# Kernel tuning notes

Hardware: AMD Instinct MI355X
Metric: run time of the kernel (lower is better)

## Reference

```python
import jax, jax.numpy as jnp
import numpy as np

# SMPL kinematic tree, first 22 joints (root has parent -1)
PARENTS = [-1, 0, 0, 0, 1, 2, 3, 4, 5, 6, 7, 8, 9, 9, 9, 12, 13, 14, 16, 17, 18, 19]
B, L, J = 64, 2048, 22


def axis_angle_to_matrix(aa):
    """aa: (..., 3) axis-angle -> (..., 3, 3) rotation matrix (Rodrigues)."""
    sq = jnp.sum(aa * aa, axis=-1, keepdims=True)
    angle = jnp.sqrt(sq + 1e-12)
    axis = aa / angle
    x, y, z = axis[..., 0], axis[..., 1], axis[..., 2]
    ang = angle[..., 0]
    c, s = jnp.cos(ang), jnp.sin(ang)
    t = 1.0 - c
    R = jnp.stack([
        t * x * x + c,     t * x * y - s * z, t * x * z + s * y,
        t * x * y + s * z, t * y * y + c,     t * y * z - s * x,
        t * x * z - s * y, t * y * z + s * x, t * z * z + c,
    ], axis=-1)
    return R.reshape(aa.shape[:-1] + (3, 3))


def get_TRS(rotmat, pos):
    """rotmat (...,3,3), pos (...,3) -> homogeneous (...,4,4)."""
    top = jnp.concatenate([rotmat, pos[..., :, None]], axis=-1)  # (...,3,4)
    bottom = jnp.broadcast_to(
        jnp.array([0.0, 0.0, 0.0, 1.0], rotmat.dtype), top.shape[:-2] + (1, 4))
    return jnp.concatenate([top, bottom], axis=-2)


def forward_kinematics(mat, parents):
    """mat: (B,L,J,4,4) local transforms -> global transforms via parent chain."""
    out = [mat[:, :, 0]]
    for j in range(1, mat.shape[2]):
        out.append(out[parents[j]] @ mat[:, :, j])
    return jnp.stack(out, axis=2)


def setup_inputs() -> dict:
    key = jax.random.key(0)
    ks = jax.random.split(key, 6)
    return {
        "body_pose": 0.3 * jax.random.normal(ks[0], (B, L, 63), jnp.float32),
        "betas": jax.random.normal(ks[1], (B, L, 10), jnp.float32),
        "global_orient": 0.3 * jax.random.normal(ks[2], (B, L, 3), jnp.float32),
        "transl": jax.random.normal(ks[3], (B, L, 3), jnp.float32),
        "J_template": jax.random.normal(ks[4], (J, 3), jnp.float32),
        "J_shapedirs": 0.01 * jax.random.normal(ks[5], (J, 3, 10), jnp.float32),
    }


def reference(body_pose, betas, global_orient, transl, J_template, J_shapedirs):
    Bm, Lm = body_pose.shape[:2]
    # (B,L,22,3) axis-angle: global orient + 21 body joints
    aa = jnp.concatenate([global_orient, body_pose], axis=-1).reshape(Bm, Lm, -1, 3)
    rotmat = axis_angle_to_matrix(aa)                                  # (B,L,22,3,3)
    skeleton = J_template[None, None] + jnp.einsum('blk,jck->bljc', betas, J_shapedirs)
    # local offsets: child - parent, root keeps its own position (+ transl)
    parent_idx = jnp.array([0] + PARENTS[1:])
    local = skeleton - skeleton[:, :, parent_idx]
    local = local.at[:, :, 0].set(skeleton[:, :, 0] + transl)
    mat = get_TRS(rotmat, local)                                       # (B,L,22,4,4)
    fk_mat = forward_kinematics(mat, PARENTS)                          # (B,L,22,4,4)
    joints = fk_mat[..., :3, 3]                                        # (B,L,22,3)
    return joints
```

## Files before the change

### kernel.cpp

```cpp
#include <hip/hip_runtime.h>

#define NT 128
#define NJ 22

struct X9 { float r[9]; float t[3]; };

__device__ __forceinline__ void rodrigues(float ax, float ay, float az, float* R) {
    float sq   = ax*ax + ay*ay + az*az + 1e-12f;
    float rinv = rsqrtf(sq);
    float ang  = sq * rinv;
    float s, c;
    __sincosf(ang, &s, &c);
    float x = ax*rinv, y = ay*rinv, z = az*rinv;
    float t = 1.0f - c;
    R[0] = t*x*x + c;   R[1] = t*x*y - s*z; R[2] = t*x*z + s*y;
    R[3] = t*x*y + s*z; R[4] = t*y*y + c;   R[5] = t*y*z - s*x;
    R[6] = t*x*z - s*y; R[7] = t*y*z + s*x; R[8] = t*z*z + c;
}

__device__ __forceinline__ void local_pos(int j, const float* bt,
                                          const float* LT, const float4* LD4,
                                          float* lt) {
    #pragma unroll
    for (int c = 0; c < 3; ++c) {
        float v = LT[j*3 + c];
        const float4 a0 = LD4[(j*3 + c)*3 + 0];
        const float4 a1 = LD4[(j*3 + c)*3 + 1];
        const float4 a2 = LD4[(j*3 + c)*3 + 2];
        v = fmaf(bt[0], a0.x, v); v = fmaf(bt[1], a0.y, v);
        v = fmaf(bt[2], a0.z, v); v = fmaf(bt[3], a0.w, v);
        v = fmaf(bt[4], a1.x, v); v = fmaf(bt[5], a1.y, v);
        v = fmaf(bt[6], a1.z, v); v = fmaf(bt[7], a1.w, v);
        v = fmaf(bt[8], a2.x, v); v = fmaf(bt[9], a2.y, v);
        lt[c] = v;
    }
}

template<int J>
__device__ __forceinline__ X9 step(const X9& gp, float* bp, const float* bt,
                                   const float* LT, const float4* LD4) {
    float R[9];
    rodrigues(bp[(J-1)*3 + 0], bp[(J-1)*3 + 1], bp[(J-1)*3 + 2], R);
    float lt[3];
    local_pos(J, bt, LT, LD4, lt);
    X9 g;
    #pragma unroll
    for (int r = 0; r < 3; ++r) {
        #pragma unroll
        for (int c = 0; c < 3; ++c)
            g.r[r*3+c] = fmaf(gp.r[r*3+0], R[c],
                         fmaf(gp.r[r*3+1], R[3+c],
                              gp.r[r*3+2] * R[6+c]));
        g.t[r] = fmaf(gp.r[r*3+0], lt[0],
                 fmaf(gp.r[r*3+1], lt[1],
                 fmaf(gp.r[r*3+2], lt[2], gp.t[r])));
    }
    bp[(J-1)*3+0] = g.t[0]; bp[(J-1)*3+1] = g.t[1]; bp[(J-1)*3+2] = g.t[2];
    return g;
}

__global__ __launch_bounds__(NT) void fk_joints_kernel(
    const float* __restrict__ body_pose,
    const float* __restrict__ betas,
    const float* __restrict__ global_orient,
    const float* __restrict__ transl,
    const float* __restrict__ J_template,
    const float* __restrict__ J_shapedirs,
    float* __restrict__ out)
{
    __shared__ float  s_bp[NT*63];
    __shared__ float  s_bt[NT*10];
    __shared__ float  s_go[NT*3];
    __shared__ float  s_tr[NT*3];
    __shared__ float  s_LT[NJ*3];
    __shared__ float4 s_LD4[NJ*3*3];

    const int tid = threadIdx.x;
    const long long s0 = (long long)blockIdx.x * NT;

    {
        const float4* src = reinterpret_cast<const float4*>(body_pose + s0*63);
        float4* dst = reinterpret_cast<float4*>(s_bp);
        #pragma unroll 4
        for (int i = tid; i < NT*63/4; i += NT) dst[i] = src[i];
    }
    {
        const float4* src = reinterpret_cast<const float4*>(betas + s0*10);
        float4* dst = reinterpret_cast<float4*>(s_bt);
        for (int i = tid; i < NT*10/4; i += NT) dst[i] = src[i];
    }
    {
        const float4* src = reinterpret_cast<const float4*>(global_orient + s0*3);
        float4* dst = reinterpret_cast<float4*>(s_go);
        if (tid < NT*3/4) dst[tid] = src[tid];
    }
    {
        const float4* src = reinterpret_cast<const float4*>(transl + s0*3);
        float4* dst = reinterpret_cast<float4*>(s_tr);
        if (tid < NT*3/4) dst[tid] = src[tid];
    }

    const int P[NJ] = {0,0,0,0,1,2,3,4,5,6,7,8,9,9,9,12,13,14,16,17,18,19};
    float* s_LD = reinterpret_cast<float*>(s_LD4);
    for (int i = tid; i < NJ*3; i += NT) {
        int j = i/3, c = i - j*3;
        float v = J_template[i];
        if (j) v -= J_template[P[j]*3 + c];
        s_LT[i] = v;
        s_LD[i*12 + 10] = 0.0f;
        s_LD[i*12 + 11] = 0.0f;
    }
    for (int i = tid; i < NJ*30; i += NT) {
        int jc = i/10, k = i - jc*10;
        int j = jc/3,  c = jc - j*3;
        float v = J_shapedirs[i];
        if (j) v -= J_shapedirs[(P[j]*3 + c)*10 + k];
        s_LD[jc*12 + k] = v;
    }
    __syncthreads();

    float bt[10];
    #pragma unroll
    for (int k = 0; k < 10; ++k) bt[k] = s_bt[tid*10 + k];

    float* bp = &s_bp[tid*63];

    X9 g0;
    rodrigues(s_go[tid*3+0], s_go[tid*3+1], s_go[tid*3+2], g0.r);
    {
        float lt0[3];
        local_pos(0, bt, s_LT, s_LD4, lt0);
        g0.t[0] = lt0[0] + s_tr[tid*3+0];
        g0.t[1] = lt0[1] + s_tr[tid*3+1];
        g0.t[2] = lt0[2] + s_tr[tid*3+2];
        s_go[tid*3+0] = g0.t[0]; s_go[tid*3+1] = g0.t[1]; s_go[tid*3+2] = g0.t[2];
    }

    X9 g;
    g = step<1 >(g0, bp, bt, s_LT, s_LD4);
    g = step<4 >(g,  bp, bt, s_LT, s_LD4);
    g = step<7 >(g,  bp, bt, s_LT, s_LD4);
    g = step<10>(g,  bp, bt, s_LT, s_LD4);
    g = step<2 >(g0, bp, bt, s_LT, s_LD4);
    g = step<5 >(g,  bp, bt, s_LT, s_LD4);
    g = step<8 >(g,  bp, bt, s_LT, s_LD4);
    g = step<11>(g,  bp, bt, s_LT, s_LD4);
    g = step<3 >(g0, bp, bt, s_LT, s_LD4);
    g = step<6 >(g,  bp, bt, s_LT, s_LD4);
    X9 g9 = step<9>(g, bp, bt, s_LT, s_LD4);
    g = step<12>(g9, bp, bt, s_LT, s_LD4);
    g = step<15>(g,  bp, bt, s_LT, s_LD4);
    g = step<13>(g9, bp, bt, s_LT, s_LD4);
    g = step<16>(g,  bp, bt, s_LT, s_LD4);
    g = step<18>(g,  bp, bt, s_LT, s_LD4);
    g = step<20>(g,  bp, bt, s_LT, s_LD4);
    g = step<14>(g9, bp, bt, s_LT, s_LD4);
    g = step<17>(g,  bp, bt, s_LT, s_LD4);
    g = step<19>(g,  bp, bt, s_LT, s_LD4);
    g = step<21>(g,  bp, bt, s_LT, s_LD4);

    __syncthreads();

    {
        float4* dst = reinterpret_cast<float4*>(out + s0 * (NJ*3));
        const int TOT4 = NT*NJ*3/4;
        for (int i = tid; i < TOT4; i += NT) {
            const int f0 = i*4;
            float v[4];
            #pragma unroll
            for (int q = 0; q < 4; ++q) {
                int f = f0 + q;
                int s = f / 66;
                int r = f - s*66;
                v[q] = (r < 3) ? s_go[s*3 + r] : s_bp[s*63 + (r - 3)];
            }
            dst[i] = make_float4(v[0], v[1], v[2], v[3]);
        }
    }
}

extern "C" void kernel_launch(void* const* d_in, const int* in_sizes, int n_in,
                              void* d_out, int out_size, void* d_ws, size_t ws_size,
                              hipStream_t stream) {
    const float* body_pose     = (const float*)d_in[0];
    const float* betas         = (const float*)d_in[1];
    const float* global_orient = (const float*)d_in[2];
    const float* transl        = (const float*)d_in[3];
    const float* J_template    = (const float*)d_in[4];
    const float* J_shapedirs   = (const float*)d_in[5];
    float* out = (float*)d_out;

    const int S = in_sizes[0] / 63;
    const int blocks = S / NT;

    hipLaunchKernelGGL(fk_joints_kernel, dim3(blocks), dim3(NT), 0, stream,
                       body_pose, betas, global_orient, transl,
                       J_template, J_shapedirs, out);
}
```

Measured before the change: 35.68 us.

## Reuse one shared buffer, hold poses in registers, write output contiguously

Shared memory is cut to a single NT*66 buffer that is reused over three phases. Body pose is staged there first and pulled into 63 registers per thread. The buffer then stages betas, global orient and translation, and finally holds the joint outputs in the exact output layout, so the epilogue becomes a plain float4 copy with no per-element div/mod gather. Launch bounds ask for 2 blocks per SM. The goal is lower LDS usage and simpler stores, paid for with extra barriers and high register pressure from the 63-element array, which may spill.

```diff
diff --git a/kernel.cpp b/kernel.cpp
--- a/kernel.cpp
+++ b/kernel.cpp
@@ -37,10 +37,10 @@
 }
 
 template<int J>
-__device__ __forceinline__ X9 step(const X9& gp, float* bp, const float* bt,
-                                   const float* LT, const float4* LD4) {
+__device__ __forceinline__ X9 step(const X9& gp, const float* aa, const float* bt,
+                                   const float* LT, const float4* LD4, float* s_o) {
     float R[9];
-    rodrigues(bp[(J-1)*3 + 0], bp[(J-1)*3 + 1], bp[(J-1)*3 + 2], R);
+    rodrigues(aa[(J-1)*3 + 0], aa[(J-1)*3 + 1], aa[(J-1)*3 + 2], R);
     float lt[3];
     local_pos(J, bt, LT, LD4, lt);
     X9 g;
@@ -55,11 +55,11 @@
                  fmaf(gp.r[r*3+1], lt[1],
                  fmaf(gp.r[r*3+2], lt[2], gp.t[r])));
     }
-    bp[(J-1)*3+0] = g.t[0]; bp[(J-1)*3+1] = g.t[1]; bp[(J-1)*3+2] = g.t[2];
+    s_o[J*3+0] = g.t[0]; s_o[J*3+1] = g.t[1]; s_o[J*3+2] = g.t[2];
     return g;
 }
 
-__global__ __launch_bounds__(NT) void fk_joints_kernel(
+__global__ __launch_bounds__(NT, 2) void fk_joints_kernel(
     const float* __restrict__ body_pose,
     const float* __restrict__ betas,
     const float* __restrict__ global_orient,
@@ -68,10 +68,7 @@
     const float* __restrict__ J_shapedirs,
     float* __restrict__ out)
 {
-    __shared__ float  s_bp[NT*63];
-    __shared__ float  s_bt[NT*10];
-    __shared__ float  s_go[NT*3];
-    __shared__ float  s_tr[NT*3];
+    __shared__ float  s_buf[NT*66];
     __shared__ float  s_LT[NJ*3];
     __shared__ float4 s_LD4[NJ*3*3];
 
@@ -80,26 +77,9 @@
 
     {
         const float4* src = reinterpret_cast<const float4*>(body_pose + s0*63);
-        float4* dst = reinterpret_cast<float4*>(s_bp);
-        #pragma unroll 4
+        float4* dst = reinterpret_cast<float4*>(s_buf);
         for (int i = tid; i < NT*63/4; i += NT) dst[i] = src[i];
     }
-    {
-        const float4* src = reinterpret_cast<const float4*>(betas + s0*10);
-        float4* dst = reinterpret_cast<float4*>(s_bt);
-        for (int i = tid; i < NT*10/4; i += NT) dst[i] = src[i];
-    }
-    {
-        const float4* src = reinterpret_cast<const float4*>(global_orient + s0*3);
-        float4* dst = reinterpret_cast<float4*>(s_go);
-        if (tid < NT*3/4) dst[tid] = src[tid];
-    }
-    {
-        const float4* src = reinterpret_cast<const float4*>(transl + s0*3);
-        float4* dst = reinterpret_cast<float4*>(s_tr);
-        if (tid < NT*3/4) dst[tid] = src[tid];
-    }
-
     const int P[NJ] = {0,0,0,0,1,2,3,4,5,6,7,8,9,9,9,12,13,14,16,17,18,19};
     float* s_LD = reinterpret_cast<float*>(s_LD4);
     for (int i = tid; i < NJ*3; i += NT) {
@@ -119,63 +99,81 @@
     }
     __syncthreads();
 
+    float aa[63];
+    #pragma unroll
+    for (int k = 0; k < 63; ++k) aa[k] = s_buf[tid*63 + k];
+    __syncthreads();
+
+    {
+        const float4* src = reinterpret_cast<const float4*>(betas + s0*10);
+        float4* dst = reinterpret_cast<float4*>(s_buf);
+        for (int i = tid; i < NT*10/4; i += NT) dst[i] = src[i];
+    }
+    {
+        const float4* src = reinterpret_cast<const float4*>(global_orient + s0*3);
+        float4* dst = reinterpret_cast<float4*>(s_buf + NT*10);
+        if (tid < NT*3/4) dst[tid] = src[tid];
+    }
+    {
+        const float4* src = reinterpret_cast<const float4*>(transl + s0*3);
+        float4* dst = reinterpret_cast<float4*>(s_buf + NT*13);
+        if (tid < NT*3/4) dst[tid] = src[tid];
+    }
+    __syncthreads();
+
     float bt[10];
     #pragma unroll
-    for (int k = 0; k < 10; ++k) bt[k] = s_bt[tid*10 + k];
+    for (int k = 0; k < 10; ++k) bt[k] = s_buf[tid*10 + k];
+    const float gox = s_buf[NT*10 + tid*3 + 0];
+    const float goy = s_buf[NT*10 + tid*3 + 1];
+    const float goz = s_buf[NT*10 + tid*3 + 2];
+    const float trx = s_buf[NT*13 + tid*3 + 0];
+    const float try_ = s_buf[NT*13 + tid*3 + 1];
+    const float trz = s_buf[NT*13 + tid*3 + 2];
+    __syncthreads();
 
-    float* bp = &s_bp[tid*63];
+    float* s_o = &s_buf[tid*66];
 
     X9 g0;
-    rodrigues(s_go[tid*3+0], s_go[tid*3+1], s_go[tid*3+2], g0.r);
+    rodrigues(gox, goy, goz, g0.r);
     {
         float lt0[3];
         local_pos(0, bt, s_LT, s_LD4, lt0);
-        g0.t[0] = lt0[0] + s_tr[tid*3+0];
-        g0.t[1] = lt0[1] + s_tr[tid*3+1];
-        g0.t[2] = lt0[2] + s_tr[tid*3+2];
-        s_go[tid*3+0] = g0.t[0]; s_go[tid*3+1] = g0.t[1]; s_go[tid*3+2] = g0.t[2];
+        g0.t[0] = lt0[0] + trx;
+        g0.t[1] = lt0[1] + try_;
+        g0.t[2] = lt0[2] + trz;
+        s_o[0] = g0.t[0]; s_o[1] = g0.t[1]; s_o[2] = g0.t[2];
     }
 
     X9 g;
-    g = step<1 >(g0, bp, bt, s_LT, s_LD4);
-    g = step<4 >(g,  bp, bt, s_LT, s_LD4);
-    g = step<7 >(g,  bp, bt, s_LT, s_LD4);
-    g = step<10>(g,  bp, bt, s_LT, s_LD4);
-    g = step<2 >(g0, bp, bt, s_LT, s_LD4);
-    g = step<5 >(g,  bp, bt, s_LT, s_LD4);
-    g = step<8 >(g,  bp, bt, s_LT, s_LD4);
-    g = step<11>(g,  bp, bt, s_LT, s_LD4);
-    g = step<3 >(g0, bp, bt, s_LT, s_LD4);
-    g = step<6 >(g,  bp, bt, s_LT, s_LD4);
-    X9 g9 = step<9>(g, bp, bt, s_LT, s_LD4);
-    g = step<12>(g9, bp, bt, s_LT, s_LD4);
-    g = step<15>(g,  bp, bt, s_LT, s_LD4);
-    g = step<13>(g9, bp, bt, s_LT, s_LD4);
-    g = step<16>(g,  bp, bt, s_LT, s_LD4);
-    g = step<18>(g,  bp, bt, s_LT, s_LD4);
-    g = step<20>(g,  bp, bt, s_LT, s_LD4);
-    g = step<14>(g9, bp, bt, s_LT, s_LD4);
-    g = step<17>(g,  bp, bt, s_LT, s_LD4);
-    g = step<19>(g,  bp, bt, s_LT, s_LD4);
-    g = step<21>(g,  bp, bt, s_LT, s_LD4);
+    g = step<1 >(g0, aa, bt, s_LT, s_LD4, s_o);
+    g = step<4 >(g,  aa, bt, s_LT, s_LD4, s_o);
+    g = step<7 >(g,  aa, bt, s_LT, s_LD4, s_o);
+    g = step<10>(g,  aa, bt, s_LT, s_LD4, s_o);
+    g = step<2 >(g0, aa, bt, s_LT, s_LD4, s_o);
+    g = step<5 >(g,  aa, bt, s_LT, s_LD4, s_o);
+    g = step<8 >(g,  aa, bt, s_LT, s_LD4, s_o);
+    g = step<11>(g,  aa, bt, s_LT, s_LD4, s_o);
+    g = step<3 >(g0, aa, bt, s_LT, s_LD4, s_o);
+    g = step<6 >(g,  aa, bt, s_LT, s_LD4, s_o);
+    X9 g9 = step<9>(g, aa, bt, s_LT, s_LD4, s_o);
+    g = step<12>(g9, aa, bt, s_LT, s_LD4, s_o);
+    g = step<15>(g,  aa, bt, s_LT, s_LD4, s_o);
+    g = step<13>(g9, aa, bt, s_LT, s_LD4, s_o);
+    g = step<16>(g,  aa, bt, s_LT, s_LD4, s_o);
+    g = step<18>(g,  aa, bt, s_LT, s_LD4, s_o);
+    g = step<20>(g,  aa, bt, s_LT, s_LD4, s_o);
+    g = step<14>(g9, aa, bt, s_LT, s_LD4, s_o);
+    g = step<17>(g,  aa, bt, s_LT, s_LD4, s_o);
+    g = step<19>(g,  aa, bt, s_LT, s_LD4, s_o);
+    g = step<21>(g,  aa, bt, s_LT, s_LD4, s_o);
 
     __syncthreads();
 
     {
+        const float4* src = reinterpret_cast<const float4*>(s_buf);
         float4* dst = reinterpret_cast<float4*>(out + s0 * (NJ*3));
-        const int TOT4 = NT*NJ*3/4;
-        for (int i = tid; i < TOT4; i += NT) {
-            const int f0 = i*4;
-            float v[4];
-            #pragma unroll
-            for (int q = 0; q < 4; ++q) {
-                int f = f0 + q;
-                int s = f / 66;
-                int r = f - s*66;
-                v[q] = (r < 3) ? s_go[s*3 + r] : s_bp[s*63 + (r - 3)];
-            }
-            dst[i] = make_float4(v[0], v[1], v[2], v[3]);
-        }
+        for (int i = tid; i < NT*NJ*3/4; i += NT) dst[i] = src[i];
     }
 }
 
```

Result: faster. 29.30 us (-17.9%).
